# Optimization experiments

Measured on AMD Instinct MI355X. Metric: run time of the kernel, lower is better.

The kernel has to match this reference:

```python
import jax, jax.numpy as jnp
import numpy as np

B, LQ, LK, D, H = 4, 2048, 2048, 768, 12
DH = D // H  # 64
EPS = 1e-5


def setup_inputs() -> dict:
    key = jax.random.key(0)
    ks = jax.random.split(key, 12)
    s = 0.02
    return {
        "queries": jax.random.normal(ks[0], (B, LQ, D), jnp.float32),
        "keys": jax.random.normal(ks[1], (B, LK, D), jnp.float32),
        "values": jax.random.normal(ks[2], (B, LK, D), jnp.float32),
        "mask": jax.random.randint(ks[3], (B, LK), 0, 2, jnp.int32),
        "Wq": jax.random.normal(ks[4], (D, D), jnp.float32) * s,
        "Wk": jax.random.normal(ks[5], (D, D), jnp.float32) * s,
        "Wv": jax.random.normal(ks[6], (D, D), jnp.float32) * s,
        "Wo": jax.random.normal(ks[7], (D, D), jnp.float32) * s,
        "W1": jax.random.normal(ks[8], (D, D), jnp.float32) * s,
        "b1": jnp.zeros((D,), jnp.float32),
        "W2": jax.random.normal(ks[9], (D, D), jnp.float32) * s,
        "b2": jnp.zeros((D,), jnp.float32),
        "ln_g": jnp.ones((D,), jnp.float32),
        "ln_b": jnp.zeros((D,), jnp.float32),
    }


def _split_heads(x):
    # [B, L, D] -> [B, H, L, DH]
    b, l, _ = x.shape
    return x.reshape(b, l, H, DH).transpose(0, 2, 1, 3)


def reference(queries, keys, values, mask, Wq, Wk, Wv, Wo, W1, b1, W2, b2, ln_g, ln_b):
    q = _split_heads(queries @ Wq)  # [B,H,LQ,DH]
    k = _split_heads(keys @ Wk)     # [B,H,LK,DH]
    v = _split_heads(values @ Wv)   # [B,H,LK,DH]

    scores = jnp.einsum("bhqd,bhkd->bhqk", q, k) / jnp.sqrt(jnp.float32(DH))

    # valid length per batch row = count of nonzero mask entries; positions >= valid_len are masked
    valid_lens = jnp.sum(mask != 0, axis=1)  # [B]
    key_ok = jnp.arange(LK, dtype=jnp.int32)[None, :] < valid_lens[:, None]  # [B,LK]
    scores = jnp.where(key_ok[:, None, None, :], scores, jnp.float32(-1e6))

    attn = jax.nn.softmax(scores, axis=-1)  # dropout is identity in eval
    out = jnp.einsum("bhqk,bhkd->bhqd", attn, v)  # [B,H,LQ,DH]
    out = out.transpose(0, 2, 1, 3).reshape(out.shape[0], out.shape[2], D)

    att_out = out @ Wo  # [B,LQ,D]
    ffn = jax.nn.relu(att_out @ W1 + b1) @ W2 + b2

    # residual + layernorm (torch code intends ln(dropout(ffn) + att_out))
    y = ffn + att_out
    mu = jnp.mean(y, axis=-1, keepdims=True)
    var = jnp.mean(jnp.square(y - mu), axis=-1, keepdims=True)
    return (y - mu) / jnp.sqrt(var + EPS) * ln_g + ln_b
```

## Files before the change

### kernel.cpp

```cpp
#include <hip/hip_runtime.h>
#include <stdint.h>

typedef __attribute__((ext_vector_type(4))) float floatx4;
typedef __attribute__((ext_vector_type(8))) __bf16 bf16x8;
typedef __attribute__((ext_vector_type(4))) short short4v;

#define DEV __device__ __forceinline__

constexpr int HB = 12;
constexpr int LSEQ = 2048;
constexpr int DMODEL = 768;
constexpr int MROWS = 8192;
constexpr float QSCALE = 0.125f * 1.44269504088896f;

DEV short f2bf(float f) {
  union { float f; uint32_t u; } x; x.f = f;
  uint32_t r = x.u + 0x7FFFu + ((x.u >> 16) & 1u);
  return (short)(r >> 16);
}

DEV float bf2f(short s) {
  union { uint32_t u; float f; } x; x.u = ((uint32_t)(uint16_t)s) << 16;
  return x.f;
}

typedef __attribute__((address_space(1))) void as1_void;
typedef __attribute__((address_space(3))) void as3_void;

DEV void gload_lds16(const void* g, void* l) {
  __builtin_amdgcn_global_load_lds((as1_void*)(uintptr_t)g, (as3_void*)l, 16, 0, 0);
}

__global__ __launch_bounds__(256)
void transpose_k(const float* w0, const float* w1, const float* w2,
                 const float* w3, const float* w4, const float* w5,
                 short* o0, short* o1, short* o2, short* o3, short* o4, short* o5)
{
  const float* W; short* O;
  switch (blockIdx.z) {
    case 0: W = w0; O = o0; break;
    case 1: W = w1; O = o1; break;
    case 2: W = w2; O = o2; break;
    case 3: W = w3; O = o3; break;
    case 4: W = w4; O = o4; break;
    default: W = w5; O = o5; break;
  }
  __shared__ float t[32][33];
  const int tx = threadIdx.x & 31, ty = threadIdx.x >> 5;
  const int n0 = blockIdx.x * 32, k0 = blockIdx.y * 32;
#pragma unroll
  for (int i = 0; i < 4; ++i)
    t[ty + i * 8][tx] = W[(size_t)(k0 + ty + i * 8) * DMODEL + n0 + tx];
  __syncthreads();
#pragma unroll
  for (int i = 0; i < 4; ++i)
    O[(size_t)(n0 + ty + i * 8) * DMODEL + k0 + tx] = f2bf(t[tx][ty + i * 8]);
}

__global__ __launch_bounds__(256)
void cvt_k(const float* __restrict__ s0, const float* __restrict__ s1, const float* __restrict__ s2,
           short* __restrict__ d0, short* __restrict__ d1, short* __restrict__ d2)
{
  const float* s; short* d;
  switch (blockIdx.y) { case 0: s = s0; d = d0; break; case 1: s = s1; d = d1; break; default: s = s2; d = d2; break; }
  const size_t i = ((size_t)blockIdx.x * 256 + threadIdx.x) * 4;
  const float4 v = *(const float4*)(s + i);
  short4 r; r.x = f2bf(v.x); r.y = f2bf(v.y); r.z = f2bf(v.z); r.w = f2bf(v.w);
  *(short4*)(d + i) = r;
}

__global__ __launch_bounds__(256)
void vlens_k(const int* __restrict__ mask, int* __restrict__ vl)
{
  const int b = blockIdx.x;
  int s = 0;
  for (int i = threadIdx.x; i < LSEQ; i += 256) s += (mask[b * LSEQ + i] != 0) ? 1 : 0;
#pragma unroll
  for (int o = 32; o >= 1; o >>= 1) s += __shfl_xor(s, o);
  __shared__ int red[4];
  const int lane = threadIdx.x & 63, wave = threadIdx.x >> 6;
  if (lane == 0) red[wave] = s;
  __syncthreads();
  if (threadIdx.x == 0) vl[b] = red[0] + red[1] + red[2] + red[3];
}

enum { EPI_QKV = 0, EPI_PLAIN = 2, EPI_BIAS_RELU = 3, EPI_Y = 4 };

template <int EPI>
__global__ __launch_bounds__(256)
void gemm_k(const short* __restrict__ A0, const short* __restrict__ A1, const short* __restrict__ A2,
            const short* __restrict__ B0, const short* __restrict__ B1, const short* __restrict__ B2,
            const float* __restrict__ bias, const short* __restrict__ resid,
            void* __restrict__ o0, void* __restrict__ o1, void* __restrict__ o2)
{
  __shared__ __align__(16) short As[2][2][64 * 32];
  __shared__ __align__(16) short Bs[2][2][128 * 32];
  const short* A = A0;
  const short* Bt = B0;
  if constexpr (EPI == EPI_QKV) {
    if (blockIdx.z == 1) { A = A1; Bt = B1; }
    else if (blockIdx.z == 2) { A = A2; Bt = B2; }
  }
  const int tid = threadIdx.x;
  const int lane = tid & 63, wave = tid >> 6;
  const int wm = wave >> 1, wn = wave & 1;
  const int m0 = blockIdx.x * 64, n0 = blockIdx.y * 128;
  const int col = lane & 15, quad = lane >> 4;
  const int sr = lane >> 2;
  const int sk = (lane & 3) * 8;

  const short* Arow = A + (size_t)(m0 + wave * 16 + sr) * DMODEL + sk;
  const short* Brow0 = Bt + (size_t)(n0 + (wave * 2 + 0) * 16 + sr) * DMODEL + sk;
  const short* Brow1 = Bt + (size_t)(n0 + (wave * 2 + 1) * 16 + sr) * DMODEL + sk;

  auto stage = [&](int kt, int buf) {
    const int k0 = kt * 64;
#pragma unroll
    for (int h = 0; h < 2; ++h) {
      gload_lds16(Arow + k0 + h * 32, &As[buf][h][wave * 512]);
      gload_lds16(Brow0 + k0 + h * 32, &Bs[buf][h][(wave * 2 + 0) * 512]);
      gload_lds16(Brow1 + k0 + h * 32, &Bs[buf][h][(wave * 2 + 1) * 512]);
    }
  };

  floatx4 acc[2][4] = {};

  stage(0, 0);
  for (int kt = 0; kt < 12; ++kt) {
    const int cur = kt & 1;
    asm volatile("s_barrier" ::: "memory");
    if (kt + 1 < 12) {
      stage(kt + 1, cur ^ 1);
      asm volatile("s_waitcnt vmcnt(6)" ::: "memory");
    } else {
      asm volatile("s_waitcnt vmcnt(0)" ::: "memory");
    }
    asm volatile("s_barrier" ::: "memory");
#pragma unroll
    for (int h = 0; h < 2; ++h) {
      bf16x8 af[2], bfr[4];
#pragma unroll
      for (int t = 0; t < 2; ++t)
        af[t] = *(const bf16x8*)&As[cur][h][(wm * 32 + t * 16 + col) * 32 + quad * 8];
#pragma unroll
      for (int t = 0; t < 4; ++t)
        bfr[t] = *(const bf16x8*)&Bs[cur][h][(wn * 64 + t * 16 + col) * 32 + quad * 8];
#pragma unroll
      for (int mt = 0; mt < 2; ++mt)
#pragma unroll
        for (int nt = 0; nt < 4; ++nt)
          acc[mt][nt] = __builtin_amdgcn_mfma_f32_16x16x32_bf16(af[mt], bfr[nt], acc[mt][nt], 0, 0, 0);
    }
  }

#pragma unroll
  for (int mt = 0; mt < 2; ++mt) {
#pragma unroll
    for (int nt = 0; nt < 4; ++nt) {
#pragma unroll
      for (int r = 0; r < 4; ++r) {
        const int m = m0 + wm * 32 + mt * 16 + quad * 4 + r;
        const int n = n0 + wn * 64 + nt * 16 + col;
        float v = acc[mt][nt][r];
        if constexpr (EPI == EPI_QKV) {
          const int b = m >> 11, l = m & 2047, h = n >> 6, dh = n & 63;
          const int z = blockIdx.z;
          if (z == 0) {
            ((short*)o0)[((size_t)(b * HB + h) * LSEQ + l) * 64 + dh] = f2bf(v * QSCALE);
          } else if (z == 1) {
            ((short*)o1)[((size_t)(b * HB + h) * LSEQ + l) * 64 + dh] = f2bf(v);
          } else {
            ((short*)o2)[((size_t)(b * HB + h) * 64 + dh) * LSEQ + l] = f2bf(v);
          }
        } else if constexpr (EPI == EPI_PLAIN) {
          ((short*)o0)[(size_t)m * DMODEL + n] = f2bf(v);
        } else if constexpr (EPI == EPI_BIAS_RELU) {
          v += bias[n]; v = v > 0.f ? v : 0.f;
          ((short*)o0)[(size_t)m * DMODEL + n] = f2bf(v);
        } else {
          v += bias[n] + bf2f(resid[(size_t)m * DMODEL + n]);
          ((float*)o0)[(size_t)m * DMODEL + n] = v;
        }
      }
    }
  }
}

__global__ __launch_bounds__(256)
void attn_k(const short* __restrict__ qw, const short* __restrict__ kw, const short* __restrict__ vtw,
            const int* __restrict__ vlens, short* __restrict__ outp)
{
  __shared__ __align__(16) short Ks[2][2][64][32];
  __shared__ __align__(16) short Vts[2][2][64][32];

  const int tid = threadIdx.x;
  const int lane = tid & 63, wave = tid >> 6;
  const int col = lane & 15, quad = lane >> 4;
  const int bh = blockIdx.x, b = bh / HB, h = bh % HB;
  const int q0 = blockIdx.y * 128;
  const int vl = vlens[b];
  const int sr = lane >> 2, sk = (lane & 3) * 8;
  const int skv = ((lane & 3) ^ ((lane >> 3) & 3)) * 8;
  const int swz = (col >> 1) & 3;

  const short* qbase = qw  + (size_t)bh * LSEQ * 64;
  const short* kbase = kw  + (size_t)bh * LSEQ * 64;
  const short* vbase = vtw + (size_t)bh * 64 * LSEQ;

  bf16x8 qf[2][2];
#pragma unroll
  for (int ks = 0; ks < 2; ++ks)
#pragma unroll
    for (int qc = 0; qc < 2; ++qc)
      qf[ks][qc] = *(const bf16x8*)(qbase + (size_t)(q0 + wave * 32 + qc * 16 + col) * 64 + ks * 32 + quad * 8);

  auto stage = [&](int kt, int buf) {
#pragma unroll
    for (int i = 0; i < 2; ++i) {
      const int c = wave * 2 + i;
      const int hs = c >> 2, r0 = (c & 3) * 16;
      gload_lds16(kbase + (size_t)(kt * 64 + r0 + sr) * 64 + hs * 32 + sk, &Ks[buf][hs][r0][0]);
      gload_lds16(vbase + (size_t)(r0 + sr) * LSEQ + kt * 64 + hs * 32 + skv, &Vts[buf][hs][r0][0]);
    }
  };

  floatx4 oacc[4][2] = {};
  float li[2] = {};

  const int ktend = (vl > 0) ? ((vl + 63) >> 6) : (LSEQ / 64);

  stage(0, 0);
  for (int kt = 0; kt < ktend; ++kt) {
    const int cur = kt & 1;
    asm volatile("s_barrier" ::: "memory");
    if (kt + 1 < ktend) {
      stage(kt + 1, cur ^ 1);
      asm volatile("s_waitcnt vmcnt(4)" ::: "memory");
    } else {
      asm volatile("s_waitcnt vmcnt(0)" ::: "memory");
    }
    asm volatile("s_barrier" ::: "memory");

    floatx4 sacc[4][2] = {};
#pragma unroll
    for (int ks = 0; ks < 2; ++ks) {
      bf16x8 kf[4];
#pragma unroll
      for (int kc = 0; kc < 4; ++kc)
        kf[kc] = *(const bf16x8*)&Ks[cur][ks][kc * 16 + col][quad * 8];
#pragma unroll
      for (int kc = 0; kc < 4; ++kc)
#pragma unroll
        for (int qc = 0; qc < 2; ++qc)
          sacc[kc][qc] = __builtin_amdgcn_mfma_f32_16x16x32_bf16(kf[kc], qf[ks][qc], sacc[kc][qc], 0, 0, 0);
    }

    if (kt * 64 + 64 > vl) {
#pragma unroll
      for (int kc = 0; kc < 4; ++kc) {
        const int pbase = kt * 64 + kc * 16 + quad * 4;
#pragma unroll
        for (int r = 0; r < 4; ++r) {
          const bool ok = (pbase + r) < vl;
#pragma unroll
          for (int qc = 0; qc < 2; ++qc)
            sacc[kc][qc][r] = ok ? sacc[kc][qc][r] : -1.0e6f;
        }
      }
    }

    short4v pf[4][2];
#pragma unroll
    for (int kc = 0; kc < 4; ++kc)
#pragma unroll
      for (int qc = 0; qc < 2; ++qc) {
        union { float f; uint32_t u; } p0, p1, p2, p3;
        p0.f = __builtin_amdgcn_exp2f(sacc[kc][qc][0]);
        p1.f = __builtin_amdgcn_exp2f(sacc[kc][qc][1]);
        p2.f = __builtin_amdgcn_exp2f(sacc[kc][qc][2]);
        p3.f = __builtin_amdgcn_exp2f(sacc[kc][qc][3]);
        li[qc] += (p0.f + p1.f) + (p2.f + p3.f);
        union { int2 i2; short4v s4; } pk;
        pk.i2.x = (int)__builtin_amdgcn_perm(p1.u, p0.u, 0x07060302u);
        pk.i2.y = (int)__builtin_amdgcn_perm(p3.u, p2.u, 0x07060302u);
        pf[kc][qc] = pk.s4;
      }

#pragma unroll
    for (int nt = 0; nt < 4; ++nt) {
      short4v vf[4];
#pragma unroll
      for (int kc = 0; kc < 4; ++kc) {
        const int jb = (((kc & 1) * 2 + (quad >> 1)) ^ swz);
        vf[kc] = *(const short4v*)&Vts[cur][kc >> 1][nt * 16 + col][jb * 8 + (quad & 1) * 4];
      }
#pragma unroll
      for (int qc = 0; qc < 2; ++qc)
#pragma unroll
        for (int kc = 0; kc < 4; ++kc)
          oacc[nt][qc] = __builtin_amdgcn_mfma_f32_16x16x16bf16_1k(vf[kc], pf[kc][qc], oacc[nt][qc], 0, 0, 0);
    }
  }

  float rli[2];
#pragma unroll
  for (int qc = 0; qc < 2; ++qc) {
    float t = li[qc];
    t += __shfl_xor(t, 16);
    t += __shfl_xor(t, 32);
    rli[qc] = 1.0f / fmaxf(t, 1e-30f);
  }

#pragma unroll
  for (int qc = 0; qc < 2; ++qc) {
    const int q = q0 + wave * 32 + qc * 16 + col;
    short* orow = outp + ((size_t)b * LSEQ + q) * DMODEL + h * 64 + quad * 4;
#pragma unroll
    for (int nt = 0; nt < 4; ++nt) {
      short4 s;
      s.x = f2bf(oacc[nt][qc][0] * rli[qc]);
      s.y = f2bf(oacc[nt][qc][1] * rli[qc]);
      s.z = f2bf(oacc[nt][qc][2] * rli[qc]);
      s.w = f2bf(oacc[nt][qc][3] * rli[qc]);
      *(short4*)(orow + nt * 16) = s;
    }
  }
}

__global__ __launch_bounds__(256)
void ln_k(const float* __restrict__ y, const float* __restrict__ g, const float* __restrict__ be,
          float* __restrict__ o)
{
  const int row = blockIdx.x;
  const int tid = threadIdx.x;
  const float* yr = y + (size_t)row * DMODEL;
  float v[3];
  float s = 0.f, sq = 0.f;
#pragma unroll
  for (int i = 0; i < 3; ++i) { v[i] = yr[tid + i * 256]; s += v[i]; sq += v[i] * v[i]; }
#pragma unroll
  for (int off = 32; off >= 1; off >>= 1) { s += __shfl_xor(s, off); sq += __shfl_xor(sq, off); }
  __shared__ float red[8];
  const int lane = tid & 63, wave = tid >> 6;
  if (lane == 0) { red[wave] = s; red[4 + wave] = sq; }
  __syncthreads();
  s = red[0] + red[1] + red[2] + red[3];
  sq = red[4] + red[5] + red[6] + red[7];
  const float mu = s * (1.f / 768.f);
  const float var = sq * (1.f / 768.f) - mu * mu;
  const float rstd = rsqrtf(var + 1e-5f);
  float* orow = o + (size_t)row * DMODEL;
#pragma unroll
  for (int i = 0; i < 3; ++i) {
    const int c = tid + i * 256;
    orow[c] = (v[i] - mu) * rstd * g[c] + be[c];
  }
}

extern "C" void kernel_launch(void* const* d_in, const int* in_sizes, int n_in,
                              void* d_out, int out_size, void* d_ws, size_t ws_size,
                              hipStream_t stream)
{
  const float* queries = (const float*)d_in[0];
  const float* keys    = (const float*)d_in[1];
  const float* values  = (const float*)d_in[2];
  const int*   mask    = (const int*)d_in[3];
  const float* Wq = (const float*)d_in[4];
  const float* Wk = (const float*)d_in[5];
  const float* Wv = (const float*)d_in[6];
  const float* Wo = (const float*)d_in[7];
  const float* W1 = (const float*)d_in[8];
  const float* b1 = (const float*)d_in[9];
  const float* W2 = (const float*)d_in[10];
  const float* b2 = (const float*)d_in[11];
  const float* ln_g = (const float*)d_in[12];
  const float* ln_b = (const float*)d_in[13];

  char* ws = (char*)d_ws;
  size_t off = 0;
  auto alloc = [&](size_t bytes) -> void* {
    void* p = ws + off;
    off = (off + bytes + 255) & ~(size_t)255;
    return p;
  };
  int* vlens = (int*)alloc(256);
  short* wt[6];
  for (int i = 0; i < 6; ++i) wt[i] = (short*)alloc((size_t)DMODEL * DMODEL * 2);
  constexpr size_t SB = (size_t)MROWS * DMODEL * 2;
  short* xq  = (short*)alloc(SB);
  short* xk  = (short*)alloc(SB);
  short* xv  = (short*)alloc(SB);
  short* qw  = (short*)alloc(SB);
  short* kw  = (short*)alloc(SB);
  short* vtw = (short*)alloc(SB);
  short* attn_cat = xq;
  short* atto_bf  = xk;
  short* h1       = xv;
  float* yb       = (float*)qw;

  dim3 blk(256);
  transpose_k<<<dim3(24, 24, 6), blk, 0, stream>>>(Wq, Wk, Wv, Wo, W1, W2,
                                                   wt[0], wt[1], wt[2], wt[3], wt[4], wt[5]);
  cvt_k<<<dim3(6144, 3), blk, 0, stream>>>(queries, keys, values, xq, xk, xv);
  vlens_k<<<dim3(4), blk, 0, stream>>>(mask, vlens);
  gemm_k<EPI_QKV><<<dim3(128, 6, 3), blk, 0, stream>>>(
      xq, xk, xv, wt[0], wt[1], wt[2], nullptr, nullptr, qw, kw, vtw);
  attn_k<<<dim3(48, 16), blk, 0, stream>>>(qw, kw, vtw, vlens, attn_cat);
  gemm_k<EPI_PLAIN><<<dim3(128, 6, 1), blk, 0, stream>>>(
      attn_cat, nullptr, nullptr, wt[3], nullptr, nullptr, nullptr, nullptr,
      atto_bf, nullptr, nullptr);
  gemm_k<EPI_BIAS_RELU><<<dim3(128, 6, 1), blk, 0, stream>>>(
      atto_bf, nullptr, nullptr, wt[4], nullptr, nullptr, b1, nullptr,
      h1, nullptr, nullptr);
  gemm_k<EPI_Y><<<dim3(128, 6, 1), blk, 0, stream>>>(
      h1, nullptr, nullptr, wt[5], nullptr, nullptr, b2, atto_bf,
      yb, nullptr, nullptr);
  ln_k<<<dim3(MROWS), blk, 0, stream>>>(yb, ln_g, ln_b, (float*)d_out);
}
```

Before: 314.7 us.

## Triple-buffer GEMM K-loop with 32-wide steps and fuse mask-length into weight prep

```diff
diff --git a/kernel.cpp b/kernel.cpp
--- a/kernel.cpp
+++ b/kernel.cpp
@@ -32,12 +32,28 @@
 }
 
 __global__ __launch_bounds__(256)
-void transpose_k(const float* w0, const float* w1, const float* w2,
-                 const float* w3, const float* w4, const float* w5,
-                 short* o0, short* o1, short* o2, short* o3, short* o4, short* o5)
-{
+void prep_k(const float* w0, const float* w1, const float* w2,
+            const float* w3, const float* w4, const float* w5,
+            short* o0, short* o1, short* o2, short* o3, short* o4, short* o5,
+            const int* __restrict__ mask, int* __restrict__ vl)
+{
+  const int id = blockIdx.x;
+  if (id >= 3456) {
+    const int b = id - 3456;
+    int s = 0;
+    for (int i = threadIdx.x; i < LSEQ; i += 256) s += (mask[b * LSEQ + i] != 0) ? 1 : 0;
+#pragma unroll
+    for (int o = 32; o >= 1; o >>= 1) s += __shfl_xor(s, o);
+    __shared__ int red[4];
+    const int lane = threadIdx.x & 63, wave = threadIdx.x >> 6;
+    if (lane == 0) red[wave] = s;
+    __syncthreads();
+    if (threadIdx.x == 0) vl[b] = red[0] + red[1] + red[2] + red[3];
+    return;
+  }
+  const int slice = id / 576, rem = id % 576;
   const float* W; short* O;
-  switch (blockIdx.z) {
+  switch (slice) {
     case 0: W = w0; O = o0; break;
     case 1: W = w1; O = o1; break;
     case 2: W = w2; O = o2; break;
@@ -47,7 +63,7 @@
   }
   __shared__ float t[32][33];
   const int tx = threadIdx.x & 31, ty = threadIdx.x >> 5;
-  const int n0 = blockIdx.x * 32, k0 = blockIdx.y * 32;
+  const int n0 = (rem % 24) * 32, k0 = (rem / 24) * 32;
 #pragma unroll
   for (int i = 0; i < 4; ++i)
     t[ty + i * 8][tx] = W[(size_t)(k0 + ty + i * 8) * DMODEL + n0 + tx];
@@ -69,21 +85,6 @@
   *(short4*)(d + i) = r;
 }
 
-__global__ __launch_bounds__(256)
-void vlens_k(const int* __restrict__ mask, int* __restrict__ vl)
-{
-  const int b = blockIdx.x;
-  int s = 0;
-  for (int i = threadIdx.x; i < LSEQ; i += 256) s += (mask[b * LSEQ + i] != 0) ? 1 : 0;
-#pragma unroll
-  for (int o = 32; o >= 1; o >>= 1) s += __shfl_xor(s, o);
-  __shared__ int red[4];
-  const int lane = threadIdx.x & 63, wave = threadIdx.x >> 6;
-  if (lane == 0) red[wave] = s;
-  __syncthreads();
-  if (threadIdx.x == 0) vl[b] = red[0] + red[1] + red[2] + red[3];
-}
-
 enum { EPI_QKV = 0, EPI_PLAIN = 2, EPI_BIAS_RELU = 3, EPI_Y = 4 };
 
 template <int EPI>
@@ -93,8 +94,8 @@
             const float* __restrict__ bias, const short* __restrict__ resid,
             void* __restrict__ o0, void* __restrict__ o1, void* __restrict__ o2)
 {
-  __shared__ __align__(16) short As[2][2][64 * 32];
-  __shared__ __align__(16) short Bs[2][2][128 * 32];
+  __shared__ __align__(16) short As[3][64 * 32];
+  __shared__ __align__(16) short Bs[3][128 * 32];
   const short* A = A0;
   const short* Bt = B0;
   if constexpr (EPI == EPI_QKV) {
@@ -114,43 +115,43 @@
   const short* Brow1 = Bt + (size_t)(n0 + (wave * 2 + 1) * 16 + sr) * DMODEL + sk;
 
   auto stage = [&](int kt, int buf) {
-    const int k0 = kt * 64;
-#pragma unroll
-    for (int h = 0; h < 2; ++h) {
-      gload_lds16(Arow + k0 + h * 32, &As[buf][h][wave * 512]);
-      gload_lds16(Brow0 + k0 + h * 32, &Bs[buf][h][(wave * 2 + 0) * 512]);
-      gload_lds16(Brow1 + k0 + h * 32, &Bs[buf][h][(wave * 2 + 1) * 512]);
-    }
+    const int k0 = kt * 32;
+    gload_lds16(Arow + k0, &As[buf][wave * 512]);
+    gload_lds16(Brow0 + k0, &Bs[buf][(wave * 2 + 0) * 512]);
+    gload_lds16(Brow1 + k0, &Bs[buf][(wave * 2 + 1) * 512]);
   };
 
   floatx4 acc[2][4] = {};
 
   stage(0, 0);
-  for (int kt = 0; kt < 12; ++kt) {
-    const int cur = kt & 1;
+  stage(1, 1);
+  int cur = 0;
+  for (int kt = 0; kt < 24; ++kt) {
     asm volatile("s_barrier" ::: "memory");
-    if (kt + 1 < 12) {
-      stage(kt + 1, cur ^ 1);
+    if (kt < 22) {
+      stage(kt + 2, cur == 0 ? 2 : cur - 1);
       asm volatile("s_waitcnt vmcnt(6)" ::: "memory");
+    } else if (kt == 22) {
+      asm volatile("s_waitcnt vmcnt(3)" ::: "memory");
     } else {
       asm volatile("s_waitcnt vmcnt(0)" ::: "memory");
     }
     asm volatile("s_barrier" ::: "memory");
-#pragma unroll
-    for (int h = 0; h < 2; ++h) {
-      bf16x8 af[2], bfr[4];
-#pragma unroll
-      for (int t = 0; t < 2; ++t)
-        af[t] = *(const bf16x8*)&As[cur][h][(wm * 32 + t * 16 + col) * 32 + quad * 8];
-#pragma unroll
-      for (int t = 0; t < 4; ++t)
-        bfr[t] = *(const bf16x8*)&Bs[cur][h][(wn * 64 + t * 16 + col) * 32 + quad * 8];
-#pragma unroll
-      for (int mt = 0; mt < 2; ++mt)
-#pragma unroll
-        for (int nt = 0; nt < 4; ++nt)
-          acc[mt][nt] = __builtin_amdgcn_mfma_f32_16x16x32_bf16(af[mt], bfr[nt], acc[mt][nt], 0, 0, 0);
-    }
+
+    bf16x8 af[2], bfr[4];
+#pragma unroll
+    for (int t = 0; t < 2; ++t)
+      af[t] = *(const bf16x8*)&As[cur][(wm * 32 + t * 16 + col) * 32 + quad * 8];
+#pragma unroll
+    for (int t = 0; t < 4; ++t)
+      bfr[t] = *(const bf16x8*)&Bs[cur][(wn * 64 + t * 16 + col) * 32 + quad * 8];
+#pragma unroll
+    for (int mt = 0; mt < 2; ++mt)
+#pragma unroll
+      for (int nt = 0; nt < 4; ++nt)
+        acc[mt][nt] = __builtin_amdgcn_mfma_f32_16x16x32_bf16(af[mt], bfr[nt], acc[mt][nt], 0, 0, 0);
+
+    cur = (cur == 2) ? 0 : cur + 1;
   }
 
 #pragma unroll
@@ -399,10 +400,10 @@
   float* yb       = (float*)qw;
 
   dim3 blk(256);
-  transpose_k<<<dim3(24, 24, 6), blk, 0, stream>>>(Wq, Wk, Wv, Wo, W1, W2,
-                                                   wt[0], wt[1], wt[2], wt[3], wt[4], wt[5]);
+  prep_k<<<dim3(3460), blk, 0, stream>>>(Wq, Wk, Wv, Wo, W1, W2,
+                                         wt[0], wt[1], wt[2], wt[3], wt[4], wt[5],
+                                         mask, vlens);
   cvt_k<<<dim3(6144, 3), blk, 0, stream>>>(queries, keys, values, xq, xk, xv);
-  vlens_k<<<dim3(4), blk, 0, stream>>>(mask, vlens);
   gemm_k<EPI_QKV><<<dim3(128, 6, 3), blk, 0, stream>>>(
       xq, xk, xv, wt[0], wt[1], wt[2], nullptr, nullptr, qw, kw, vtw);
   attn_k<<<dim3(48, 16), blk, 0, stream>>>(qw, kw, vtw, vlens, attn_cat);
```

Result: slower. 335.5 us (+6.6%).

## Merge prep kernels into one launch and halve attention query tile

Applied to the files above, without the earlier changes.

```diff
diff --git a/kernel.cpp b/kernel.cpp
--- a/kernel.cpp
+++ b/kernel.cpp
@@ -32,12 +32,41 @@
 }
 
 __global__ __launch_bounds__(256)
-void transpose_k(const float* w0, const float* w1, const float* w2,
-                 const float* w3, const float* w4, const float* w5,
-                 short* o0, short* o1, short* o2, short* o3, short* o4, short* o5)
+void prep_k(const float* w0, const float* w1, const float* w2,
+            const float* w3, const float* w4, const float* w5,
+            short* o0, short* o1, short* o2, short* o3, short* o4, short* o5,
+            const int* __restrict__ mask, int* __restrict__ vl,
+            const float* __restrict__ aq, const float* __restrict__ ak, const float* __restrict__ av,
+            short* __restrict__ dq, short* __restrict__ dk, short* __restrict__ dv)
 {
+  const int id = blockIdx.x;
+  if (id >= 3460) {
+    const int cid = id - 3460;
+    const int t = cid / 6144, inner = cid % 6144;
+    const float* s = (t == 0) ? aq : (t == 1) ? ak : av;
+    short* d = (t == 0) ? dq : (t == 1) ? dk : dv;
+    const size_t i = ((size_t)inner * 256 + threadIdx.x) * 4;
+    const float4 v = *(const float4*)(s + i);
+    short4 r; r.x = f2bf(v.x); r.y = f2bf(v.y); r.z = f2bf(v.z); r.w = f2bf(v.w);
+    *(short4*)(d + i) = r;
+    return;
+  }
+  if (id >= 3456) {
+    const int b = id - 3456;
+    int s = 0;
+    for (int i = threadIdx.x; i < LSEQ; i += 256) s += (mask[b * LSEQ + i] != 0) ? 1 : 0;
+#pragma unroll
+    for (int o = 32; o >= 1; o >>= 1) s += __shfl_xor(s, o);
+    __shared__ int red[4];
+    const int lane = threadIdx.x & 63, wave = threadIdx.x >> 6;
+    if (lane == 0) red[wave] = s;
+    __syncthreads();
+    if (threadIdx.x == 0) vl[b] = red[0] + red[1] + red[2] + red[3];
+    return;
+  }
+  const int slice = id / 576, rem = id % 576;
   const float* W; short* O;
-  switch (blockIdx.z) {
+  switch (slice) {
     case 0: W = w0; O = o0; break;
     case 1: W = w1; O = o1; break;
     case 2: W = w2; O = o2; break;
@@ -47,7 +76,7 @@
   }
   __shared__ float t[32][33];
   const int tx = threadIdx.x & 31, ty = threadIdx.x >> 5;
-  const int n0 = blockIdx.x * 32, k0 = blockIdx.y * 32;
+  const int n0 = (rem % 24) * 32, k0 = (rem / 24) * 32;
 #pragma unroll
   for (int i = 0; i < 4; ++i)
     t[ty + i * 8][tx] = W[(size_t)(k0 + ty + i * 8) * DMODEL + n0 + tx];
@@ -55,33 +84,6 @@
 #pragma unroll
   for (int i = 0; i < 4; ++i)
     O[(size_t)(n0 + ty + i * 8) * DMODEL + k0 + tx] = f2bf(t[tx][ty + i * 8]);
-}
-
-__global__ __launch_bounds__(256)
-void cvt_k(const float* __restrict__ s0, const float* __restrict__ s1, const float* __restrict__ s2,
-           short* __restrict__ d0, short* __restrict__ d1, short* __restrict__ d2)
-{
-  const float* s; short* d;
-  switch (blockIdx.y) { case 0: s = s0; d = d0; break; case 1: s = s1; d = d1; break; default: s = s2; d = d2; break; }
-  const size_t i = ((size_t)blockIdx.x * 256 + threadIdx.x) * 4;
-  const float4 v = *(const float4*)(s + i);
-  short4 r; r.x = f2bf(v.x); r.y = f2bf(v.y); r.z = f2bf(v.z); r.w = f2bf(v.w);
-  *(short4*)(d + i) = r;
-}
-
-__global__ __launch_bounds__(256)
-void vlens_k(const int* __restrict__ mask, int* __restrict__ vl)
-{
-  const int b = blockIdx.x;
-  int s = 0;
-  for (int i = threadIdx.x; i < LSEQ; i += 256) s += (mask[b * LSEQ + i] != 0) ? 1 : 0;
-#pragma unroll
-  for (int o = 32; o >= 1; o >>= 1) s += __shfl_xor(s, o);
-  __shared__ int red[4];
-  const int lane = threadIdx.x & 63, wave = threadIdx.x >> 6;
-  if (lane == 0) red[wave] = s;
-  __syncthreads();
-  if (threadIdx.x == 0) vl[b] = red[0] + red[1] + red[2] + red[3];
 }
 
 enum { EPI_QKV = 0, EPI_PLAIN = 2, EPI_BIAS_RELU = 3, EPI_Y = 4 };
@@ -197,7 +199,7 @@
   const int lane = tid & 63, wave = tid >> 6;
   const int col = lane & 15, quad = lane >> 4;
   const int bh = blockIdx.x, b = bh / HB, h = bh % HB;
-  const int q0 = blockIdx.y * 128;
+  const int q0 = blockIdx.y * 64;
   const int vl = vlens[b];
   const int sr = lane >> 2, sk = (lane & 3) * 8;
   const int skv = ((lane & 3) ^ ((lane >> 3) & 3)) * 8;
@@ -207,12 +209,10 @@
   const short* kbase = kw  + (size_t)bh * LSEQ * 64;
   const short* vbase = vtw + (size_t)bh * 64 * LSEQ;
 
-  bf16x8 qf[2][2];
+  bf16x8 qf[2];
 #pragma unroll
   for (int ks = 0; ks < 2; ++ks)
-#pragma unroll
-    for (int qc = 0; qc < 2; ++qc)
-      qf[ks][qc] = *(const bf16x8*)(qbase + (size_t)(q0 + wave * 32 + qc * 16 + col) * 64 + ks * 32 + quad * 8);
+    qf[ks] = *(const bf16x8*)(qbase + (size_t)(q0 + wave * 16 + col) * 64 + ks * 32 + quad * 8);
 
   auto stage = [&](int kt, int buf) {
 #pragma unroll
@@ -224,8 +224,8 @@
     }
   };
 
-  floatx4 oacc[4][2] = {};
-  float li[2] = {};
+  floatx4 oacc[4] = {};
+  float li = 0.f;
 
   const int ktend = (vl > 0) ? ((vl + 63) >> 6) : (LSEQ / 64);
 
@@ -241,7 +241,7 @@
     }
     asm volatile("s_barrier" ::: "memory");
 
-    floatx4 sacc[4][2] = {};
+    floatx4 sacc[4] = {};
 #pragma unroll
     for (int ks = 0; ks < 2; ++ks) {
       bf16x8 kf[4];
@@ -250,9 +250,7 @@
         kf[kc] = *(const bf16x8*)&Ks[cur][ks][kc * 16 + col][quad * 8];
 #pragma unroll
       for (int kc = 0; kc < 4; ++kc)
-#pragma unroll
-        for (int qc = 0; qc < 2; ++qc)
-          sacc[kc][qc] = __builtin_amdgcn_mfma_f32_16x16x32_bf16(kf[kc], qf[ks][qc], sacc[kc][qc], 0, 0, 0);
+        sacc[kc] = __builtin_amdgcn_mfma_f32_16x16x32_bf16(kf[kc], qf[ks], sacc[kc], 0, 0, 0);
     }
 
     if (kt * 64 + 64 > vl) {
@@ -262,29 +260,25 @@
 #pragma unroll
         for (int r = 0; r < 4; ++r) {
           const bool ok = (pbase + r) < vl;
-#pragma unroll
-          for (int qc = 0; qc < 2; ++qc)
-            sacc[kc][qc][r] = ok ? sacc[kc][qc][r] : -1.0e6f;
+          sacc[kc][r] = ok ? sacc[kc][r] : -1.0e6f;
         }
       }
     }
 
-    short4v pf[4][2];
-#pragma unroll
-    for (int kc = 0; kc < 4; ++kc)
-#pragma unroll
-      for (int qc = 0; qc < 2; ++qc) {
-        union { float f; uint32_t u; } p0, p1, p2, p3;
-        p0.f = __builtin_amdgcn_exp2f(sacc[kc][qc][0]);
-        p1.f = __builtin_amdgcn_exp2f(sacc[kc][qc][1]);
-        p2.f = __builtin_amdgcn_exp2f(sacc[kc][qc][2]);
-        p3.f = __builtin_amdgcn_exp2f(sacc[kc][qc][3]);
-        li[qc] += (p0.f + p1.f) + (p2.f + p3.f);
-        union { int2 i2; short4v s4; } pk;
-        pk.i2.x = (int)__builtin_amdgcn_perm(p1.u, p0.u, 0x07060302u);
-        pk.i2.y = (int)__builtin_amdgcn_perm(p3.u, p2.u, 0x07060302u);
-        pf[kc][qc] = pk.s4;
-      }
+    short4v pf[4];
+#pragma unroll
+    for (int kc = 0; kc < 4; ++kc) {
+      union { float f; uint32_t u; } p0, p1, p2, p3;
+      p0.f = __builtin_amdgcn_exp2f(sacc[kc][0]);
+      p1.f = __builtin_amdgcn_exp2f(sacc[kc][1]);
+      p2.f = __builtin_amdgcn_exp2f(sacc[kc][2]);
+      p3.f = __builtin_amdgcn_exp2f(sacc[kc][3]);
+      li += (p0.f + p1.f) + (p2.f + p3.f);
+      union { int2 i2; short4v s4; } pk;
+      pk.i2.x = (int)__builtin_amdgcn_perm(p1.u, p0.u, 0x07060302u);
+      pk.i2.y = (int)__builtin_amdgcn_perm(p3.u, p2.u, 0x07060302u);
+      pf[kc] = pk.s4;
+    }
 
 #pragma unroll
     for (int nt = 0; nt < 4; ++nt) {
@@ -295,35 +289,26 @@
         vf[kc] = *(const short4v*)&Vts[cur][kc >> 1][nt * 16 + col][jb * 8 + (quad & 1) * 4];
       }
 #pragma unroll
-      for (int qc = 0; qc < 2; ++qc)
-#pragma unroll
-        for (int kc = 0; kc < 4; ++kc)
-          oacc[nt][qc] = __builtin_amdgcn_mfma_f32_16x16x16bf16_1k(vf[kc], pf[kc][qc], oacc[nt][qc], 0, 0, 0);
-    }
-  }
-
-  float rli[2];
-#pragma unroll
-  for (int qc = 0; qc < 2; ++qc) {
-    float t = li[qc];
-    t += __shfl_xor(t, 16);
-    t += __shfl_xor(t, 32);
-    rli[qc] = 1.0f / fmaxf(t, 1e-30f);
-  }
-
-#pragma unroll
-  for (int qc = 0; qc < 2; ++qc) {
-    const int q = q0 + wave * 32 + qc * 16 + col;
-    short* orow = outp + ((size_t)b * LSEQ + q) * DMODEL + h * 64 + quad * 4;
-#pragma unroll
-    for (int nt = 0; nt < 4; ++nt) {
-      short4 s;
-      s.x = f2bf(oacc[nt][qc][0] * rli[qc]);
-      s.y = f2bf(oacc[nt][qc][1] * rli[qc]);
-      s.z = f2bf(oacc[nt][qc][2] * rli[qc]);
-      s.w = f2bf(oacc[nt][qc][3] * rli[qc]);
-      *(short4*)(orow + nt * 16) = s;
-    }
+      for (int kc = 0; kc < 4; ++kc)
+        oacc[nt] = __builtin_amdgcn_mfma_f32_16x16x16bf16_1k(vf[kc], pf[kc], oacc[nt], 0, 0, 0);
+    }
+  }
+
+  float t = li;
+  t += __shfl_xor(t, 16);
+  t += __shfl_xor(t, 32);
+  const float rli = 1.0f / fmaxf(t, 1e-30f);
+
+  const int q = q0 + wave * 16 + col;
+  short* orow = outp + ((size_t)b * LSEQ + q) * DMODEL + h * 64 + quad * 4;
+#pragma unroll
+  for (int nt = 0; nt < 4; ++nt) {
+    short4 s;
+    s.x = f2bf(oacc[nt][0] * rli);
+    s.y = f2bf(oacc[nt][1] * rli);
+    s.z = f2bf(oacc[nt][2] * rli);
+    s.w = f2bf(oacc[nt][3] * rli);
+    *(short4*)(orow + nt * 16) = s;
   }
 }
 
@@ -399,13 +384,13 @@
   float* yb       = (float*)qw;
 
   dim3 blk(256);
-  transpose_k<<<dim3(24, 24, 6), blk, 0, stream>>>(Wq, Wk, Wv, Wo, W1, W2,
-                                                   wt[0], wt[1], wt[2], wt[3], wt[4], wt[5]);
-  cvt_k<<<dim3(6144, 3), blk, 0, stream>>>(queries, keys, values, xq, xk, xv);
-  vlens_k<<<dim3(4), blk, 0, stream>>>(mask, vlens);
+  prep_k<<<dim3(21892), blk, 0, stream>>>(Wq, Wk, Wv, Wo, W1, W2,
+                                          wt[0], wt[1], wt[2], wt[3], wt[4], wt[5],
+                                          mask, vlens,
+                                          queries, keys, values, xq, xk, xv);
   gemm_k<EPI_QKV><<<dim3(128, 6, 3), blk, 0, stream>>>(
       xq, xk, xv, wt[0], wt[1], wt[2], nullptr, nullptr, qw, kw, vtw);
-  attn_k<<<dim3(48, 16), blk, 0, stream>>>(qw, kw, vtw, vlens, attn_cat);
+  attn_k<<<dim3(48, 32), blk, 0, stream>>>(qw, kw, vtw, vlens, attn_cat);
   gemm_k<EPI_PLAIN><<<dim3(128, 6, 1), blk, 0, stream>>>(
       attn_cat, nullptr, nullptr, wt[3], nullptr, nullptr, nullptr, nullptr,
       atto_bf, nullptr, nullptr);
```

Measured after the change: 309.8 us. No clear change (-1.6%).
